# Kernel tuning notes

Measured on AMD Instinct MI355X. Metric: run time of the kernel, lower is better.

The kernel has to match this reference:

```python
import jax, jax.numpy as jnp
import numpy as np

B, T, C, H = 2, 2048, 1024, 16
D = C // H


def setup_inputs() -> dict:
    key = jax.random.key(0)
    k1, k2, k3 = jax.random.split(key, 3)
    x = jax.random.normal(k1, (B, T, C), dtype=jnp.float32)
    w_attn = jax.random.normal(k2, (3 * C, C), dtype=jnp.float32) * (1.0 / np.sqrt(C))
    w_proj = jax.random.normal(k3, (C, C), dtype=jnp.float32) * (1.0 / np.sqrt(C))
    # causal mask, 1 = keep, 0 = masked (matches att.masked_fill(mask == 0, -inf))
    mask = jnp.tril(jnp.ones((T, T), dtype=jnp.int32))[None, None, :, :]
    return {"x": x, "w_attn": w_attn, "w_proj": w_proj, "mask": mask}


def reference(x, w_attn, w_proj, mask):
    Bq, Tq, Cq = x.shape
    qkv = x @ w_attn.T                      # [B,T,3C] (torch Linear: x @ W^T)
    q, k, v = jnp.split(qkv, 3, axis=2)
    # [B,T,C] -> [B,H,T,D]
    q = q.reshape(Bq, Tq, H, D).transpose(0, 2, 1, 3)
    k = k.reshape(Bq, Tq, H, D).transpose(0, 2, 1, 3)
    v = v.reshape(Bq, Tq, H, D).transpose(0, 2, 1, 3)
    att = jnp.einsum("bhqd,bhkd->bhqk", q, k) * (1.0 / np.sqrt(D))
    att = jnp.where(mask == 0, -jnp.inf, att)
    att = jax.nn.softmax(att, axis=-1)      # dropout p=0.0 -> identity
    y = jnp.einsum("bhqk,bhkd->bhqd", att, v)
    y = y.transpose(0, 2, 1, 3).reshape(Bq, Tq, Cq)
    return y @ w_proj.T
```

## Files before the change

### kernel.cpp

```cpp
#include <hip/hip_runtime.h>
#include <hip/hip_bf16.h>
#include <math.h>


typedef __attribute__((ext_vector_type(4))) float floatx4;
typedef __attribute__((ext_vector_type(8))) __bf16 bf16x8;
typedef __attribute__((ext_vector_type(4))) __bf16 bf16x4;
typedef __attribute__((ext_vector_type(4))) short short4v;

#define MFMA_BF16(a, b, c) __builtin_amdgcn_mfma_f32_16x16x32_bf16((a), (b), (c), 0, 0, 0)

#if __has_builtin(__builtin_amdgcn_mfma_f32_16x16x16bf16_1k)
__device__ inline floatx4 mfma16(bf16x4 a, bf16x4 b, floatx4 c) {
    union { bf16x4 h; short4v s; } ua, ub;
    ua.h = a; ub.h = b;
    return __builtin_amdgcn_mfma_f32_16x16x16bf16_1k(ua.s, ub.s, c, 0, 0, 0);
}
#else
__device__ inline floatx4 mfma16(bf16x4 a, bf16x4 b, floatx4 c) {
    const bf16x4 z = {};
    return MFMA_BF16(__builtin_shufflevector(a, z, 0, 1, 2, 3, 4, 5, 6, 7),
                     __builtin_shufflevector(b, z, 0, 1, 2, 3, 4, 5, 6, 7), c);
}
#endif

typedef __attribute__((address_space(1))) const uint32_t* gas_t;
typedef __attribute__((address_space(3))) uint32_t* las_t;
__device__ inline void gl2lds16(const void* g, void* l) {
    __builtin_amdgcn_global_load_lds((gas_t)g, (las_t)l, 16, 0, 0);
}

__device__ inline uint4 cvt8_f32_bf16(const float4 a, const float4 b) {
    union { __hip_bfloat16 h[8]; uint4 u; } c;
    c.h[0] = __float2bfloat16(a.x); c.h[1] = __float2bfloat16(a.y);
    c.h[2] = __float2bfloat16(a.z); c.h[3] = __float2bfloat16(a.w);
    c.h[4] = __float2bfloat16(b.x); c.h[5] = __float2bfloat16(b.y);
    c.h[6] = __float2bfloat16(b.z); c.h[7] = __float2bfloat16(b.w);
    return c.u;
}

__global__ __launch_bounds__(256) void cvt_all(
    const float* __restrict__ x, const float* __restrict__ wa,
    const float* __restrict__ wp, __hip_bfloat16* __restrict__ out)
{
    const size_t e = ((size_t)blockIdx.x * 256 + threadIdx.x) * 8;
    const float* src; size_t off;
    if (e < 4194304)      { src = x;  off = e; }
    else if (e < 7340032) { src = wa; off = e - 4194304; }
    else                  { src = wp; off = e - 7340032; }
    const float4 a = *(const float4*)&src[off];
    const float4 b = *(const float4*)&src[off + 4];
    *(uint4*)&out[e] = cvt8_f32_bf16(a, b);
}

__global__ __launch_bounds__(256) void gemm_qkv(
    const __hip_bfloat16* __restrict__ A,
    const __hip_bfloat16* __restrict__ Bt,
    __hip_bfloat16* __restrict__ qk,
    __hip_bfloat16* __restrict__ vt, int K)
{
    __shared__ __hip_bfloat16 As0[128][32];
    __shared__ __hip_bfloat16 As1[128][32];
    __shared__ __hip_bfloat16 Bs0[128][32];
    __shared__ __hip_bfloat16 Bs1[128][32];

    const int tid  = threadIdx.x;
    const int wave = tid >> 6;
    const int lane = tid & 63;
    const int quad = lane >> 4;
    const int l15  = lane & 15;
    const int wrow = wave >> 1;
    const int wcol = wave & 1;
    const int bm = blockIdx.y * 128;
    const int bn = blockIdx.x * 128;

    floatx4 acc[4][4];
#pragma unroll
    for (int i = 0; i < 4; ++i)
#pragma unroll
        for (int j = 0; j < 4; ++j)
            acc[i][j] = (floatx4){0.f, 0.f, 0.f, 0.f};

    const int srow = lane >> 2;
    const int scol = (lane & 3) * 8;

    const __hip_bfloat16* Abase = A  + (size_t)bm * K;
    const __hip_bfloat16* Bbase = Bt + (size_t)bn * K;

    for (int k0 = 0; k0 < K; k0 += 64) {
#pragma unroll
        for (int c = 0; c < 2; ++c) {
            const int rbase = wave * 32 + c * 16;
            const size_t ga = (size_t)(rbase + srow) * K + k0 + scol;
            gl2lds16(&Abase[ga],      &As0[rbase][0]);
            gl2lds16(&Abase[ga + 32], &As1[rbase][0]);
            gl2lds16(&Bbase[ga],      &Bs0[rbase][0]);
            gl2lds16(&Bbase[ga + 32], &Bs1[rbase][0]);
        }
        __syncthreads();

#pragma unroll
        for (int kd = 0; kd < 2; ++kd) {
            const __hip_bfloat16 (*Ap)[32] = kd ? As1 : As0;
            const __hip_bfloat16 (*Bp)[32] = kd ? Bs1 : Bs0;
            bf16x8 af[4], bfv[4];
#pragma unroll
            for (int i = 0; i < 4; ++i)
                af[i] = *(const bf16x8*)&Ap[wrow * 64 + i * 16 + l15][quad * 8];
#pragma unroll
            for (int j = 0; j < 4; ++j)
                bfv[j] = *(const bf16x8*)&Bp[wcol * 64 + j * 16 + l15][quad * 8];
#pragma unroll
            for (int i = 0; i < 4; ++i)
#pragma unroll
                for (int j = 0; j < 4; ++j)
                    acc[i][j] = MFMA_BF16(af[i], bfv[j], acc[i][j]);
        }
        __syncthreads();
    }

    if (bn < 2048) {
        const float sc = (bn < 1024) ? 0.18033688f : 1.0f;
#pragma unroll
        for (int i = 0; i < 4; ++i)
#pragma unroll
            for (int j = 0; j < 4; ++j)
#pragma unroll
                for (int r = 0; r < 4; ++r) {
                    const int row = bm + wrow * 64 + i * 16 + quad * 4 + r;
                    const int col = bn + wcol * 64 + j * 16 + l15;
                    qk[(size_t)row * 2048 + col] = __float2bfloat16(acc[i][j][r] * sc);
                }
    } else {
#pragma unroll
        for (int i = 0; i < 4; ++i)
#pragma unroll
            for (int j = 0; j < 4; ++j) {
                const int trow0 = bm + wrow * 64 + i * 16 + quad * 4;
                const int d = bn - 2048 + wcol * 64 + j * 16 + l15;
                const int b = trow0 >> 11, t0 = trow0 & 2047;
                union { __hip_bfloat16 h[4]; uint2 u; } pk;
#pragma unroll
                for (int r = 0; r < 4; ++r) pk.h[r] = __float2bfloat16(acc[i][j][r]);
                *(uint2*)&vt[((size_t)(b * 16 + (d >> 6)) * 64 + (d & 63)) * 2048 + t0] = pk.u;
            }
    }
}

__global__ __launch_bounds__(256) void gemm_bt_mfma_n64(
    const __hip_bfloat16* __restrict__ A,
    const __hip_bfloat16* __restrict__ Bt,
    float* __restrict__ C, int M, int N, int K)
{
    __shared__ __hip_bfloat16 As[128][32];
    __shared__ __hip_bfloat16 Bs[64][32];

    const int tid  = threadIdx.x;
    const int wave = tid >> 6;
    const int lane = tid & 63;
    const int quad = lane >> 4;
    const int l15  = lane & 15;
    const int wrow = wave >> 1;
    const int wcol = wave & 1;
    const int bm = blockIdx.y * 128;
    const int bn = blockIdx.x * 64;

    floatx4 acc[4][2];
#pragma unroll
    for (int i = 0; i < 4; ++i)
#pragma unroll
        for (int j = 0; j < 2; ++j)
            acc[i][j] = (floatx4){0.f, 0.f, 0.f, 0.f};

    const int srow = lane >> 2;
    const int scol = (lane & 3) * 8;

    const __hip_bfloat16* Abase = A  + (size_t)bm * K;
    const __hip_bfloat16* Bbase = Bt + (size_t)bn * K;

    for (int k0 = 0; k0 < K; k0 += 32) {
        {
            const int ra0 = wave * 32;
            gl2lds16(&Abase[(size_t)(ra0 + srow) * K + k0 + scol], &As[ra0][0]);
            gl2lds16(&Abase[(size_t)(ra0 + 16 + srow) * K + k0 + scol], &As[ra0 + 16][0]);
            const int rb0 = wave * 16;
            gl2lds16(&Bbase[(size_t)(rb0 + srow) * K + k0 + scol], &Bs[rb0][0]);
        }
        __syncthreads();

        bf16x8 af[4], bfv[2];
#pragma unroll
        for (int i = 0; i < 4; ++i)
            af[i] = *(const bf16x8*)&As[wrow * 64 + i * 16 + l15][quad * 8];
#pragma unroll
        for (int j = 0; j < 2; ++j)
            bfv[j] = *(const bf16x8*)&Bs[wcol * 32 + j * 16 + l15][quad * 8];

#pragma unroll
        for (int i = 0; i < 4; ++i)
#pragma unroll
            for (int j = 0; j < 2; ++j)
                acc[i][j] = MFMA_BF16(af[i], bfv[j], acc[i][j]);
        __syncthreads();
    }

#pragma unroll
    for (int i = 0; i < 4; ++i)
#pragma unroll
        for (int j = 0; j < 2; ++j)
#pragma unroll
            for (int r = 0; r < 4; ++r) {
                const int row = bm + wrow * 64 + i * 16 + quad * 4 + r;
                const int col = bn + wcol * 32 + j * 16 + l15;
                C[(size_t)row * N + col] = acc[i][j][r];
            }
}

__global__ __launch_bounds__(256) void attn_kernel(
    const __hip_bfloat16* __restrict__ qk,
    const __hip_bfloat16* __restrict__ vt,
    float* __restrict__ part)
{
    constexpr int T = 2048;
    __shared__ __hip_bfloat16 Ks[2][64][72];
    __shared__ __hip_bfloat16 Vt[2][64][72];

    const int bh = blockIdx.x;
    const int b = bh >> 4, h = bh & 15;
    const int p = blockIdx.y;
    const int s = blockIdx.z;
    const int q0A = p * 64;
    const int q0B = (31 - p) * 64;

    const int tid  = threadIdx.x;
    const int wave = tid >> 6;
    const int lane = tid & 63;
    const int quad = lane >> 4;
    const int l15  = lane & 15;

    const __hip_bfloat16* base  = qk + (size_t)b * T * 2048;
    const __hip_bfloat16* vbase = vt + (size_t)((b * 16 + h) * 64) * 2048;

    bf16x8 aqA[2], aqB[2];
#pragma unroll
    for (int kd = 0; kd < 2; ++kd) {
        aqA[kd] = *(const bf16x8*)&base[(size_t)(q0A + wave * 16 + l15) * 2048 + h * 64 + kd * 32 + quad * 8];
        aqB[kd] = *(const bf16x8*)&base[(size_t)(q0B + wave * 16 + l15) * 2048 + h * 64 + kd * 32 + quad * 8];
    }

    bf16x4 ones4;
#pragma unroll
    for (int i = 0; i < 4; ++i) ones4[i] = (__bf16)1.0f;

    floatx4 accA[4], accB[4], lTA, lTB;
#pragma unroll
    for (int r = 0; r < 4; ++r) {
        accA[r] = (floatx4){0.f, 0.f, 0.f, 0.f};
        accB[r] = (floatx4){0.f, 0.f, 0.f, 0.f};
    }
    lTA = (floatx4){0.f, 0.f, 0.f, 0.f};
    lTB = (floatx4){0.f, 0.f, 0.f, 0.f};

    const int sr = tid >> 2;
    const int sc = (tid & 3) * 16;
    const int myq = wave * 16 + l15;

    {
        const int j0 = s * 64;
        const size_t kg = (size_t)(j0 + sr) * 2048 + 1024 + h * 64 + sc;
        *(uint4*)&Ks[0][sr][sc]     = *(const uint4*)&base[kg];
        *(uint4*)&Ks[0][sr][sc + 8] = *(const uint4*)&base[kg + 8];
        const size_t vg = (size_t)sr * 2048 + j0 + sc;
        *(uint4*)&Vt[0][sr][sc]     = *(const uint4*)&vbase[vg];
        *(uint4*)&Vt[0][sr][sc + 8] = *(const uint4*)&vbase[vg + 8];
    }
    __syncthreads();

    int cur = 0;
    for (int j0 = s * 64; j0 <= q0B; j0 += 128) {
        const bool actA  = (j0 <= q0A);
        const bool dgA   = (j0 == q0A);
        const bool dgB   = (j0 == q0B);
        const bool hnext = (j0 + 128 <= q0B);

        uint4 pk0, pk1, pv0, pv1;
        if (hnext) {
            const size_t kg = (size_t)(j0 + 128 + sr) * 2048 + 1024 + h * 64 + sc;
            pk0 = *(const uint4*)&base[kg];
            pk1 = *(const uint4*)&base[kg + 8];
            const size_t vg = (size_t)sr * 2048 + (j0 + 128) + sc;
            pv0 = *(const uint4*)&vbase[vg];
            pv1 = *(const uint4*)&vbase[vg + 8];
        }

        floatx4 sA[4], sB[4];
#pragma unroll
        for (int jt = 0; jt < 4; ++jt) {
            sA[jt] = (floatx4){0.f, 0.f, 0.f, 0.f};
            sB[jt] = (floatx4){0.f, 0.f, 0.f, 0.f};
        }
#pragma unroll
        for (int jt = 0; jt < 4; ++jt)
#pragma unroll
            for (int kd = 0; kd < 2; ++kd) {
                bf16x8 ak = *(const bf16x8*)&Ks[cur][jt * 16 + l15][kd * 32 + quad * 8];
                sB[jt] = MFMA_BF16(ak, aqB[kd], sB[jt]);
                if (actA) sA[jt] = MFMA_BF16(ak, aqA[kd], sA[jt]);
            }

        bf16x4 pfA[4], pfB[4];
#pragma unroll
        for (int jt = 0; jt < 4; ++jt) {
            const int kvl = jt * 16 + quad * 4;
#pragma unroll
            for (int r = 0; r < 4; ++r) {
                float pv = __builtin_amdgcn_exp2f(sB[jt][r]);
                if (dgB && (kvl + r) > myq) pv = 0.f;
                pfB[jt][r] = (__bf16)__float2bfloat16(pv);
            }
            if (actA) {
#pragma unroll
                for (int r = 0; r < 4; ++r) {
                    float pv = __builtin_amdgcn_exp2f(sA[jt][r]);
                    if (dgA && (kvl + r) > myq) pv = 0.f;
                    pfA[jt][r] = (__bf16)__float2bfloat16(pv);
                }
            }
        }

#pragma unroll
        for (int jt = 0; jt < 4; ++jt) {
            lTB = mfma16(ones4, pfB[jt], lTB);
            if (actA) lTA = mfma16(ones4, pfA[jt], lTA);
        }

#pragma unroll
        for (int jd = 0; jd < 4; ++jd)
#pragma unroll
            for (int jt = 0; jt < 4; ++jt) {
                const bf16x4 av = *(const bf16x4*)&Vt[cur][jd * 16 + l15][jt * 16 + quad * 4];
                accB[jd] = mfma16(av, pfB[jt], accB[jd]);
                if (actA) accA[jd] = mfma16(av, pfA[jt], accA[jd]);
            }

        if (hnext) {
            const int nxt = cur ^ 1;
            *(uint4*)&Ks[nxt][sr][sc]     = pk0;
            *(uint4*)&Ks[nxt][sr][sc + 8] = pk1;
            *(uint4*)&Vt[nxt][sr][sc]     = pv0;
            *(uint4*)&Vt[nxt][sr][sc + 8] = pv1;
            __syncthreads();
        }
        cur ^= 1;
    }

    float* pA = part + (size_t)((s * 32 + bh) * 32 + p) * 4160;
    float* pB = part + (size_t)((s * 32 + bh) * 32 + (31 - p)) * 4160;
#pragma unroll
    for (int jd = 0; jd < 4; ++jd)
#pragma unroll
        for (int r = 0; r < 4; ++r) {
            const int d = jd * 16 + quad * 4 + r;
            pA[d * 64 + myq] = accA[jd][r];
            pB[d * 64 + myq] = accB[jd][r];
        }
    if (quad == 0) {
        pA[4096 + myq] = lTA[0];
        pB[4096 + myq] = lTB[0];
    }
}

__global__ __launch_bounds__(256) void combine_kernel(
    const float* __restrict__ part, __hip_bfloat16* __restrict__ y)
{
    const int bh = blockIdx.x, t = blockIdx.y;
    const int b = bh >> 4, h = bh & 15;
    const float* p0 = part + (size_t)((0 * 32 + bh) * 32 + t) * 4160;
    const float* p1 = part + (size_t)((1 * 32 + bh) * 32 + t) * 4160;

    __shared__ float Ls[64][65];
    __shared__ float linv[64];
    const int tid = threadIdx.x;
    if (tid < 64) linv[tid] = 1.f / (p0[4096 + tid] + p1[4096 + tid]);

    const int dr = tid >> 2;
    const int q0 = (tid & 3) * 16;
#pragma unroll
    for (int c = 0; c < 4; ++c) {
        const float4 a = *(const float4*)&p0[dr * 64 + q0 + c * 4];
        const float4 e = *(const float4*)&p1[dr * 64 + q0 + c * 4];
        Ls[dr][q0 + c * 4 + 0] = a.x + e.x;
        Ls[dr][q0 + c * 4 + 1] = a.y + e.y;
        Ls[dr][q0 + c * 4 + 2] = a.z + e.z;
        Ls[dr][q0 + c * 4 + 3] = a.w + e.w;
    }
    __syncthreads();

    const int q  = tid >> 2;
    const int d0 = (tid & 3) * 16;
    const float inv = linv[q];
    union { __hip_bfloat16 hh[16]; uint4 u[2]; } ob;
#pragma unroll
    for (int j = 0; j < 16; ++j)
        ob.hh[j] = __float2bfloat16(Ls[d0 + j][q] * inv);
    __hip_bfloat16* yp = &y[((size_t)(b * 2048 + t * 64 + q)) * 1024 + h * 64 + d0];
    *(uint4*)(yp)     = ob.u[0];
    *(uint4*)(yp + 8) = ob.u[1];
}

extern "C" void kernel_launch(void* const* d_in, const int* in_sizes, int n_in,
                              void* d_out, int out_size, void* d_ws, size_t ws_size,
                              hipStream_t stream)
{
    const float* x      = (const float*)d_in[0];
    const float* w_attn = (const float*)d_in[1];
    const float* w_proj = (const float*)d_in[2];

    float* out = (float*)d_out;
    __hip_bfloat16* xb  = (__hip_bfloat16*)d_ws;
    __hip_bfloat16* wab = xb  + (size_t)4096 * 1024;
    __hip_bfloat16* wpb = wab + (size_t)3072 * 1024;
    __hip_bfloat16* qkb = wpb + (size_t)1024 * 1024;
    __hip_bfloat16* y   = qkb + (size_t)4096 * 2048;
    __hip_bfloat16* vt  = y   + (size_t)4096 * 1024;
    float*          prt = (float*)(vt + (size_t)2048 * 2048);

    cvt_all<<<4096, 256, 0, stream>>>(x, w_attn, w_proj, xb);

    gemm_qkv<<<dim3(24, 32), 256, 0, stream>>>(xb, wab, qkb, vt, 1024);

    attn_kernel<<<dim3(32, 16, 2), 256, 0, stream>>>(qkb, vt, prt);
    combine_kernel<<<dim3(32, 32), 256, 0, stream>>>(prt, y);

    gemm_bt_mfma_n64<<<dim3(16, 32), 256, 0, stream>>>(y, wpb, out, 4096, 1024, 1024);
}
```

Baseline: 206.6 us.

## Stage QKV GEMM epilogue through LDS and split attention loop by active halves

The QKV GEMM epilogue now writes results into shared memory first, including the transpose for V, and then stores them to global memory as coalesced 16-byte rows instead of scattered 2-byte and 8-byte stores. The attention kernel drops its register-prefetched double buffer in favour of a single LDS buffer loaded synchronously each iteration. It also splits the loop into a phase where both query tiles are active and a B-only phase, which removes the per-iteration actA branches. Softmax probabilities are converted to bf16 with packed conversions. Losing the prefetch exposes global load latency in attention, in exchange for lower register and LDS use.

```diff
diff --git a/kernel.cpp b/kernel.cpp
--- a/kernel.cpp
+++ b/kernel.cpp
@@ -37,6 +37,13 @@
     c.h[4] = __float2bfloat16(b.x); c.h[5] = __float2bfloat16(b.y);
     c.h[6] = __float2bfloat16(b.z); c.h[7] = __float2bfloat16(b.w);
     return c.u;
+}
+
+__device__ inline bf16x4 cvt_pk4(float p0, float p1, float p2, float p3) {
+    union { __hip_bfloat162 h2[2]; bf16x4 v; } u;
+    u.h2[0] = __float22bfloat162_rn(float2{p0, p1});
+    u.h2[1] = __float22bfloat162_rn(float2{p2, p3});
+    return u.v;
 }
 
 __global__ __launch_bounds__(256) void cvt_all(
@@ -59,10 +66,11 @@
     __hip_bfloat16* __restrict__ qk,
     __hip_bfloat16* __restrict__ vt, int K)
 {
-    __shared__ __hip_bfloat16 As0[128][32];
-    __shared__ __hip_bfloat16 As1[128][32];
-    __shared__ __hip_bfloat16 Bs0[128][32];
-    __shared__ __hip_bfloat16 Bs1[128][32];
+    __shared__ __hip_bfloat16 smem[17408];
+    __hip_bfloat16 (*As0)[32] = (__hip_bfloat16(*)[32])(smem);
+    __hip_bfloat16 (*As1)[32] = (__hip_bfloat16(*)[32])(smem + 4096);
+    __hip_bfloat16 (*Bs0)[32] = (__hip_bfloat16(*)[32])(smem + 8192);
+    __hip_bfloat16 (*Bs1)[32] = (__hip_bfloat16(*)[32])(smem + 12288);
 
     const int tid  = threadIdx.x;
     const int wave = tid >> 6;
@@ -119,31 +127,50 @@
         __syncthreads();
     }
 
-    if (bn < 2048) {
+    const bool isqk = (bn < 2048);
+    if (isqk) {
         const float sc = (bn < 1024) ? 0.18033688f : 1.0f;
 #pragma unroll
         for (int i = 0; i < 4; ++i)
 #pragma unroll
-            for (int j = 0; j < 4; ++j)
-#pragma unroll
-                for (int r = 0; r < 4; ++r) {
-                    const int row = bm + wrow * 64 + i * 16 + quad * 4 + r;
-                    const int col = bn + wcol * 64 + j * 16 + l15;
-                    qk[(size_t)row * 2048 + col] = __float2bfloat16(acc[i][j][r] * sc);
-                }
+            for (int j = 0; j < 4; ++j) {
+                const int row = wrow * 64 + i * 16 + quad * 4;
+                const int col = wcol * 64 + j * 16 + l15;
+#pragma unroll
+                for (int r = 0; r < 4; ++r)
+                    smem[(row + r) * 136 + col] = __float2bfloat16(acc[i][j][r] * sc);
+            }
     } else {
 #pragma unroll
         for (int i = 0; i < 4; ++i)
 #pragma unroll
             for (int j = 0; j < 4; ++j) {
-                const int trow0 = bm + wrow * 64 + i * 16 + quad * 4;
-                const int d = bn - 2048 + wcol * 64 + j * 16 + l15;
-                const int b = trow0 >> 11, t0 = trow0 & 2047;
-                union { __hip_bfloat16 h[4]; uint2 u; } pk;
-#pragma unroll
-                for (int r = 0; r < 4; ++r) pk.h[r] = __float2bfloat16(acc[i][j][r]);
-                *(uint2*)&vt[((size_t)(b * 16 + (d >> 6)) * 64 + (d & 63)) * 2048 + t0] = pk.u;
-            }
+                const int trow = wrow * 64 + i * 16 + quad * 4;
+                const int dcol = wcol * 64 + j * 16 + l15;
+#pragma unroll
+                for (int r = 0; r < 4; ++r)
+                    smem[dcol * 136 + trow + r] = __float2bfloat16(acc[i][j][r]);
+            }
+    }
+    __syncthreads();
+
+    const int rr0 = tid >> 4;
+    const int cc  = (tid & 15) * 8;
+    if (isqk) {
+#pragma unroll
+        for (int pass = 0; pass < 8; ++pass) {
+            const int rr = pass * 16 + rr0;
+            *(uint4*)&qk[(size_t)(bm + rr) * 2048 + bn + cc] =
+                *(const uint4*)&smem[rr * 136 + cc];
+        }
+    } else {
+        const int b = bm >> 11, t0 = (bm & 2047) + cc;
+#pragma unroll
+        for (int pass = 0; pass < 8; ++pass) {
+            const int d = (bn - 2048) + pass * 16 + rr0;
+            *(uint4*)&vt[((size_t)((b * 16 + (d >> 6)) * 64 + (d & 63))) * 2048 + t0] =
+                *(const uint4*)&smem[(pass * 16 + rr0) * 136 + cc];
+        }
     }
 }
 
@@ -222,8 +249,8 @@
     float* __restrict__ part)
 {
     constexpr int T = 2048;
-    __shared__ __hip_bfloat16 Ks[2][64][72];
-    __shared__ __hip_bfloat16 Vt[2][64][72];
+    __shared__ __hip_bfloat16 Ks[64][72];
+    __shared__ __hip_bfloat16 Vt[64][72];
 
     const int bh = blockIdx.x;
     const int b = bh >> 4, h = bh & 15;
@@ -265,33 +292,21 @@
     const int sc = (tid & 3) * 16;
     const int myq = wave * 16 + l15;
 
-    {
-        const int j0 = s * 64;
-        const size_t kg = (size_t)(j0 + sr) * 2048 + 1024 + h * 64 + sc;
-        *(uint4*)&Ks[0][sr][sc]     = *(const uint4*)&base[kg];
-        *(uint4*)&Ks[0][sr][sc + 8] = *(const uint4*)&base[kg + 8];
-        const size_t vg = (size_t)sr * 2048 + j0 + sc;
-        *(uint4*)&Vt[0][sr][sc]     = *(const uint4*)&vbase[vg];
-        *(uint4*)&Vt[0][sr][sc + 8] = *(const uint4*)&vbase[vg + 8];
-    }
-    __syncthreads();
-
-    int cur = 0;
-    for (int j0 = s * 64; j0 <= q0B; j0 += 128) {
-        const bool actA  = (j0 <= q0A);
-        const bool dgA   = (j0 == q0A);
-        const bool dgB   = (j0 == q0B);
-        const bool hnext = (j0 + 128 <= q0B);
-
-        uint4 pk0, pk1, pv0, pv1;
-        if (hnext) {
-            const size_t kg = (size_t)(j0 + 128 + sr) * 2048 + 1024 + h * 64 + sc;
-            pk0 = *(const uint4*)&base[kg];
-            pk1 = *(const uint4*)&base[kg + 8];
-            const size_t vg = (size_t)sr * 2048 + (j0 + 128) + sc;
-            pv0 = *(const uint4*)&vbase[vg];
-            pv1 = *(const uint4*)&vbase[vg + 8];
-        }
+#define STAGE_TILE(J0)                                                         \
+    {                                                                          \
+        const size_t kg = (size_t)((J0) + sr) * 2048 + 1024 + h * 64 + sc;     \
+        *(uint4*)&Ks[sr][sc]     = *(const uint4*)&base[kg];                   \
+        *(uint4*)&Ks[sr][sc + 8] = *(const uint4*)&base[kg + 8];               \
+        const size_t vg = (size_t)sr * 2048 + (J0) + sc;                       \
+        *(uint4*)&Vt[sr][sc]     = *(const uint4*)&vbase[vg];                  \
+        *(uint4*)&Vt[sr][sc + 8] = *(const uint4*)&vbase[vg + 8];              \
+    }
+
+    int j0 = s * 64;
+
+    for (; j0 <= q0A; j0 += 128) {
+        STAGE_TILE(j0);
+        __syncthreads();
 
         floatx4 sA[4], sB[4];
 #pragma unroll
@@ -303,56 +318,88 @@
         for (int jt = 0; jt < 4; ++jt)
 #pragma unroll
             for (int kd = 0; kd < 2; ++kd) {
-                bf16x8 ak = *(const bf16x8*)&Ks[cur][jt * 16 + l15][kd * 32 + quad * 8];
+                bf16x8 ak = *(const bf16x8*)&Ks[jt * 16 + l15][kd * 32 + quad * 8];
                 sB[jt] = MFMA_BF16(ak, aqB[kd], sB[jt]);
-                if (actA) sA[jt] = MFMA_BF16(ak, aqA[kd], sA[jt]);
-            }
-
+                sA[jt] = MFMA_BF16(ak, aqA[kd], sA[jt]);
+            }
+
+        const bool dgA = (j0 == q0A);
         bf16x4 pfA[4], pfB[4];
 #pragma unroll
         for (int jt = 0; jt < 4; ++jt) {
             const int kvl = jt * 16 + quad * 4;
+            float pb[4], pa[4];
+#pragma unroll
+            for (int r = 0; r < 4; ++r) {
+                pb[r] = __builtin_amdgcn_exp2f(sB[jt][r]);
+                float pv = __builtin_amdgcn_exp2f(sA[jt][r]);
+                if (dgA && (kvl + r) > myq) pv = 0.f;
+                pa[r] = pv;
+            }
+            pfB[jt] = cvt_pk4(pb[0], pb[1], pb[2], pb[3]);
+            pfA[jt] = cvt_pk4(pa[0], pa[1], pa[2], pa[3]);
+        }
+
+#pragma unroll
+        for (int jt = 0; jt < 4; ++jt) {
+            lTB = mfma16(ones4, pfB[jt], lTB);
+            lTA = mfma16(ones4, pfA[jt], lTA);
+        }
+#pragma unroll
+        for (int jd = 0; jd < 4; ++jd)
+#pragma unroll
+            for (int jt = 0; jt < 4; ++jt) {
+                const bf16x4 av = *(const bf16x4*)&Vt[jd * 16 + l15][jt * 16 + quad * 4];
+                accB[jd] = mfma16(av, pfB[jt], accB[jd]);
+                accA[jd] = mfma16(av, pfA[jt], accA[jd]);
+            }
+        __syncthreads();
+    }
+
+    for (; j0 <= q0B; j0 += 128) {
+        STAGE_TILE(j0);
+        __syncthreads();
+
+        floatx4 sB[4];
+#pragma unroll
+        for (int jt = 0; jt < 4; ++jt)
+            sB[jt] = (floatx4){0.f, 0.f, 0.f, 0.f};
+#pragma unroll
+        for (int jt = 0; jt < 4; ++jt)
+#pragma unroll
+            for (int kd = 0; kd < 2; ++kd) {
+                bf16x8 ak = *(const bf16x8*)&Ks[jt * 16 + l15][kd * 32 + quad * 8];
+                sB[jt] = MFMA_BF16(ak, aqB[kd], sB[jt]);
+            }
+
+        const bool dgB = (j0 == q0B);
+        bf16x4 pfB[4];
+#pragma unroll
+        for (int jt = 0; jt < 4; ++jt) {
+            const int kvl = jt * 16 + quad * 4;
+            float pb[4];
 #pragma unroll
             for (int r = 0; r < 4; ++r) {
                 float pv = __builtin_amdgcn_exp2f(sB[jt][r]);
                 if (dgB && (kvl + r) > myq) pv = 0.f;
-                pfB[jt][r] = (__bf16)__float2bfloat16(pv);
-            }
-            if (actA) {
-#pragma unroll
-                for (int r = 0; r < 4; ++r) {
-                    float pv = __builtin_amdgcn_exp2f(sA[jt][r]);
-                    if (dgA && (kvl + r) > myq) pv = 0.f;
-                    pfA[jt][r] = (__bf16)__float2bfloat16(pv);
-                }
-            }
-        }
-
-#pragma unroll
-        for (int jt = 0; jt < 4; ++jt) {
+                pb[r] = pv;
+            }
+            pfB[jt] = cvt_pk4(pb[0], pb[1], pb[2], pb[3]);
+        }
+
+#pragma unroll
+        for (int jt = 0; jt < 4; ++jt)
             lTB = mfma16(ones4, pfB[jt], lTB);
-            if (actA) lTA = mfma16(ones4, pfA[jt], lTA);
-        }
-
 #pragma unroll
         for (int jd = 0; jd < 4; ++jd)
 #pragma unroll
             for (int jt = 0; jt < 4; ++jt) {
-                const bf16x4 av = *(const bf16x4*)&Vt[cur][jd * 16 + l15][jt * 16 + quad * 4];
+                const bf16x4 av = *(const bf16x4*)&Vt[jd * 16 + l15][jt * 16 + quad * 4];
                 accB[jd] = mfma16(av, pfB[jt], accB[jd]);
-                if (actA) accA[jd] = mfma16(av, pfA[jt], accA[jd]);
-            }
-
-        if (hnext) {
-            const int nxt = cur ^ 1;
-            *(uint4*)&Ks[nxt][sr][sc]     = pk0;
-            *(uint4*)&Ks[nxt][sr][sc + 8] = pk1;
-            *(uint4*)&Vt[nxt][sr][sc]     = pv0;
-            *(uint4*)&Vt[nxt][sr][sc + 8] = pv1;
-            __syncthreads();
-        }
-        cur ^= 1;
-    }
+            }
+        __syncthreads();
+    }
+#undef STAGE_TILE
 
     float* pA = part + (size_t)((s * 32 + bh) * 32 + p) * 4160;
     float* pB = part + (size_t)((s * 32 + bh) * 32 + (31 - p)) * 4160;
```

Result: faster. 194.9 us (-5.6%).
